# Optimization experiments

Hardware: AMD Instinct MI355X
Metric: run time of the kernel (lower is better)

## Reference

```python
import jax, jax.numpy as jnp
import numpy as np

B, N, M, C1, C2 = 16, 4096, 1024, 128, 256
MLP0, MLP1 = 256, 256
IN_CH = C1 + C2
EPS = 1e-5


def setup_inputs() -> dict:
    key = jax.random.key(0)
    ks = jax.random.split(key, 6)
    return {
        "xyz1": jax.random.normal(ks[0], (B, 3, N), jnp.float32),
        "xyz2": jax.random.normal(ks[1], (B, 3, M), jnp.float32),
        "points1": jax.random.normal(ks[2], (B, C1, N), jnp.float32),
        "points2": jax.random.normal(ks[3], (B, C2, M), jnp.float32),
        "W1": jax.random.normal(ks[4], (MLP0, IN_CH), jnp.float32) * (1.0 / np.sqrt(IN_CH)),
        "gamma1": jnp.ones((MLP0,), jnp.float32),
        "beta1": jnp.zeros((MLP0,), jnp.float32),
        "W2": jax.random.normal(ks[5], (MLP1, MLP0), jnp.float32) * (1.0 / np.sqrt(MLP0)),
        "gamma2": jnp.ones((MLP1,), jnp.float32),
        "beta2": jnp.zeros((MLP1,), jnp.float32),
    }


def _batchnorm(x, gamma, beta):
    # x: (B, N, C); normalize per channel over batch*length (training-mode BN, biased var)
    mean = jnp.mean(x, axis=(0, 1))
    var = jnp.mean((x - mean) ** 2, axis=(0, 1))
    return (x - mean) * jax.lax.rsqrt(var + EPS) * gamma + beta


def reference(xyz1, xyz2, points1, points2, W1, gamma1, beta1, W2, gamma2, beta2):
    p1 = jnp.swapaxes(xyz1, 1, 2)  # (B, N, 3)
    p2 = jnp.swapaxes(xyz2, 1, 2)  # (B, M, 3)
    # squared pairwise distances (B, N, M); squaring preserves 3-NN ordering,
    # and the original squares the euclidean dist before weighting anyway
    d2 = jnp.sum((p1[:, :, None, :] - p2[:, None, :, :]) ** 2, axis=-1)
    neg_d2, idx = jax.lax.top_k(-d2, 3)  # 3 smallest distances
    dist2 = jnp.maximum(-neg_d2, 1e-10)  # (B, N, 3)
    inv = 1.0 / dist2
    weight = inv / jnp.sum(inv, axis=-1, keepdims=True)  # (B, N, 3)
    f2 = jnp.swapaxes(points2, 1, 2)  # (B, M, C2)
    b, n, k = idx.shape
    gathered = jnp.take_along_axis(
        f2, idx.reshape(b, n * k)[:, :, None], axis=1
    ).reshape(b, n, k, -1)  # (B, N, 3, C2)
    interp = jnp.einsum("bnk,bnkc->bnc", weight, gathered)  # (B, N, C2)
    feat = jnp.concatenate([interp, jnp.swapaxes(points1, 1, 2)], axis=-1)  # (B, N, C1+C2)
    h = jnp.einsum("bnc,oc->bno", feat, W1)  # conv1d k=1, no bias
    h = jax.nn.relu(_batchnorm(h, gamma1, beta1))
    h = jnp.einsum("bnc,oc->bno", h, W2)
    h = jax.nn.relu(_batchnorm(h, gamma2, beta2))
    return jnp.swapaxes(h, 1, 2)  # (B, MLP1, N), channel-first like torch
```

## Files before the change

### kernel.cpp

```cpp
#include <hip/hip_runtime.h>

typedef unsigned short u16;
typedef unsigned int u32;

#define BB 16
#define NN 4096
#define MM 1024
#define C1V 128
#define C2V 256
#define O1 256
#define O2 256
#define EPSV 1e-5f
#define INV_CNT (1.0f/65536.0f)
#define NREP 32

typedef __attribute__((ext_vector_type(8))) short bf16x8;
typedef __attribute__((ext_vector_type(4))) float f32x4;

static __device__ __forceinline__ u16 f2b(float f) {
  u32 u = __float_as_uint(f);
  u32 r = (u + 0x7FFFu + ((u >> 16) & 1u)) >> 16;
  return (u16)r;
}
static __device__ __forceinline__ float b2f(u16 s) {
  return __uint_as_float(((u32)s) << 16);
}

#define GLD_LDS16(gp, lp)                                                      \
  __builtin_amdgcn_global_load_lds(                                            \
      (const __attribute__((address_space(1))) void*)(gp),                     \
      (__attribute__((address_space(3))) void*)(lp), 16, 0, 0)

__global__ __launch_bounds__(256) void knn_kernel(
    const float* __restrict__ xyz1, const float* __restrict__ xyz2,
    float* __restrict__ pd, int* __restrict__ pi) {
  __shared__ float4 cand[256];
  int bx = blockIdx.x;
  int c = bx & 3;
  int qt = (bx >> 2) & 7;
  int b = bx >> 5;
  int t = threadIdx.x;

  const float* x2b = xyz2 + b * 3 * MM;
  {
    float x = x2b[c * 256 + t];
    float y = x2b[MM + c * 256 + t];
    float z = x2b[2 * MM + c * 256 + t];
    cand[t] = make_float4(x, y, z, x * x + y * y + z * z);
  }
  __syncthreads();

  const float* x1b = xyz1 + b * 3 * NN;
  int n0 = qt * 512 + t;
  int n1 = n0 + 256;
  float px0 = x1b[n0], py0 = x1b[NN + n0], pz0 = x1b[2 * NN + n0];
  float px1 = x1b[n1], py1 = x1b[NN + n1], pz1 = x1b[2 * NN + n1];

  const float INF = 3.4e38f;
  float k00 = INF, k01 = INF, k02 = INF;
  float k10 = INF, k11 = INF, k12 = INF;
  int j00 = 0, j01 = 0, j02 = 0;
  int j10 = 0, j11 = 0, j12 = 0;

#pragma unroll 8
  for (int m = 0; m < 256; ++m) {
    float4 cd = cand[m];
    {
      float dot = fmaf(px0, cd.x, fmaf(py0, cd.y, pz0 * cd.z));
      float key = fmaf(-2.0f, dot, cd.w);
      bool c0 = key < k00, c1 = key < k01, c2 = key < k02;
      k02 = c1 ? k01 : (c2 ? key : k02);
      j02 = c1 ? j01 : (c2 ? m : j02);
      k01 = c0 ? k00 : (c1 ? key : k01);
      j01 = c0 ? j00 : (c1 ? m : j01);
      k00 = c0 ? key : k00;
      j00 = c0 ? m : j00;
    }
    {
      float dot = fmaf(px1, cd.x, fmaf(py1, cd.y, pz1 * cd.z));
      float key = fmaf(-2.0f, dot, cd.w);
      bool c0 = key < k10, c1 = key < k11, c2 = key < k12;
      k12 = c1 ? k11 : (c2 ? key : k12);
      j12 = c1 ? j11 : (c2 ? m : j12);
      k11 = c0 ? k10 : (c1 ? key : k11);
      j11 = c0 ? j10 : (c1 ? m : j11);
      k10 = c0 ? key : k10;
      j10 = c0 ? m : j10;
    }
  }

  float pn0 = px0 * px0 + py0 * py0 + pz0 * pz0;
  float pn1 = px1 * px1 + py1 * py1 + pz1 * pz1;
  int gq0 = b * NN + n0;
  int gq1 = b * NN + n1;
  int base = c << 8;
  ((float4*)pd)[(size_t)c * 65536 + gq0] =
      make_float4(fmaxf(k00 + pn0, 1e-10f), fmaxf(k01 + pn0, 1e-10f),
                  fmaxf(k02 + pn0, 1e-10f), 0.0f);
  ((int4*)pi)[(size_t)c * 65536 + gq0] =
      make_int4(base + j00, base + j01, base + j02, 0);
  ((float4*)pd)[(size_t)c * 65536 + gq1] =
      make_float4(fmaxf(k10 + pn1, 1e-10f), fmaxf(k11 + pn1, 1e-10f),
                  fmaxf(k12 + pn1, 1e-10f), 0.0f);
  ((int4*)pi)[(size_t)c * 65536 + gq1] =
      make_int4(base + j10, base + j11, base + j12, 0);
}

__global__ __launch_bounds__(256) void knn_merge(
    const float* __restrict__ pd, const int* __restrict__ pi,
    float* __restrict__ w_out, int* __restrict__ i_out) {
  int gq = blockIdx.x * 256 + threadIdx.x;
  float4 d0 = ((const float4*)pd)[gq];
  int4 i0 = ((const int4*)pi)[gq];
  float a0 = d0.x, a1 = d0.y, a2 = d0.z;
  int b0 = i0.x, b1 = i0.y, b2 = i0.z;
#pragma unroll
  for (int c = 1; c < 4; ++c) {
    float4 dc = ((const float4*)pd)[(size_t)c * 65536 + gq];
    int4 ic = ((const int4*)pi)[(size_t)c * 65536 + gq];
    float kv[3] = {dc.x, dc.y, dc.z};
    int jv[3] = {ic.x, ic.y, ic.z};
#pragma unroll
    for (int j = 0; j < 3; ++j) {
      float key = kv[j];
      int idx = jv[j];
      bool c0 = key < a0, c1 = key < a1, c2 = key < a2;
      a2 = c1 ? a1 : (c2 ? key : a2);
      b2 = c1 ? b1 : (c2 ? idx : b2);
      a1 = c0 ? a0 : (c1 ? key : a1);
      b1 = c0 ? b0 : (c1 ? idx : b1);
      a0 = c0 ? key : a0;
      b0 = c0 ? idx : b0;
    }
  }
  float v0 = 1.0f / a0, v1 = 1.0f / a1, v2 = 1.0f / a2;
  float s = 1.0f / (v0 + v1 + v2);
  int base = gq * 3;
  w_out[base + 0] = v0 * s;
  w_out[base + 1] = v1 * s;
  w_out[base + 2] = v2 * s;
  i_out[base + 0] = b0;
  i_out[base + 1] = b1;
  i_out[base + 2] = b2;
}

__global__ __launch_bounds__(256) void cast_w_kernel(
    const float* __restrict__ src, u16* __restrict__ dst, int n) {
  int i = blockIdx.x * 256 + threadIdx.x;
  if (i < n) dst[i] = f2b(src[i]);
}

__global__ __launch_bounds__(256) void tcast_kernel(
    const float* __restrict__ in, u16* __restrict__ out, int C, int P) {
  __shared__ float tile[32][33];
  int tx = threadIdx.x & 31, ty = threadIdx.x >> 5;
  int p0 = blockIdx.x * 32, c0 = blockIdx.y * 32, b = blockIdx.z;
  const float* ib = in + (size_t)b * C * P;
  u16* ob = out + (size_t)b * P * C;
#pragma unroll
  for (int i = 0; i < 4; ++i)
    tile[ty + i * 8][tx] = ib[(size_t)(c0 + ty + i * 8) * P + p0 + tx];
  __syncthreads();
#pragma unroll
  for (int i = 0; i < 4; ++i)
    ob[(size_t)(p0 + ty + i * 8) * C + c0 + tx] = f2b(tile[tx][ty + i * 8]);
}

__global__ __launch_bounds__(512) void stats_finalize(
    const float* __restrict__ R, float* __restrict__ outS) {
  int u = threadIdx.x;
  float s = 0.0f;
#pragma unroll
  for (int r = 0; r < NREP; ++r) s += R[r * 512 + u];
  outS[u] = s;
}

template <int K, int NTILES, bool INTERP, bool STATS, bool OUTB, bool BNA>
__global__ __launch_bounds__(256) void gemm_mfma(
    const u16* __restrict__ A, int lda, const u16* __restrict__ B, int ldb,
    void* __restrict__ out, const u16* __restrict__ G,
    const float* __restrict__ w3, const int* __restrict__ i3,
    float* __restrict__ statsOut, const float* __restrict__ statsInR,
    const float* __restrict__ gamma, const float* __restrict__ beta) {
  __shared__ u16 smem[16384];
  __shared__ float wsh[128][3];
  __shared__ int ish[128][3];
  __shared__ float scA[256], shA[256];

  int t = threadIdx.x;
  int w = t >> 6, l = t & 63;
  int n0;
  if (NTILES > 0) {
    int p = blockIdx.x;
    int batch = ((p & 7) << 1) | ((p >> 3) & 1);
    int nt = p >> 4;
    n0 = (batch * NTILES + nt) * 128;
  } else {
    n0 = blockIdx.x * 128;
  }
  int o0 = blockIdx.y * 128;

  if (INTERP) {
    for (int e = t; e < 384; e += 256) {
      int r = e / 3, j = e - 3 * r;
      wsh[r][j] = w3[(n0 + r) * 3 + j];
      ish[r][j] = i3[(n0 + r) * 3 + j];
    }
  }
  if (BNA) {
    float s = 0.0f, qq = 0.0f;
#pragma unroll
    for (int r = 0; r < NREP; ++r) {
      s += statsInR[r * 512 + t];
      qq += statsInR[r * 512 + 256 + t];
    }
    float mean = s * INV_CNT;
    float var = qq * INV_CNT - mean * mean;
    float sc = rsqrtf(var + EPSV) * gamma[t];
    scA[t] = sc;
    shA[t] = beta[t] - mean * sc;
  }

  int wm = w & 1, wn = w >> 1;
  int lr = l >> 2, lc = l & 3;
  int q = l >> 4, m = l & 15;

  f32x4 acc[4][4] = {};
  u16* As = smem;
  u16* Bs = smem + 4096;

  const u16* arow = A + (size_t)n0 * lda;
  const u16* brow = B + (size_t)o0 * ldb;

#pragma unroll
  for (int kt = 0; kt < K; kt += 32) {
    __syncthreads();
#pragma unroll
    for (int r = 0; r < 2; ++r) {
      int row = r * 64 + w * 16 + lr;
      if (BNA) {
        union { uint4 u; u16 s[8]; } v, o;
        v.u = *(const uint4*)(arow + (size_t)row * lda + kt + lc * 8);
        int cb = kt + lc * 8;
#pragma unroll
        for (int j = 0; j < 8; ++j) {
          float f = fmaf(b2f(v.s[j]), scA[cb + j], shA[cb + j]);
          o.s[j] = f2b(fmaxf(f, 0.0f));
        }
        *(uint4*)(As + row * 32 + lc * 8) = o.u;
      } else {
        GLD_LDS16(arow + (size_t)row * lda + kt + lc * 8, As + row * 32 + lc * 8);
      }
    }
#pragma unroll
    for (int r = 0; r < 2; ++r) {
      int row = r * 64 + w * 16 + lr;
      GLD_LDS16(brow + (size_t)row * ldb + kt + lc * 8, Bs + row * 32 + lc * 8);
    }
    __syncthreads();
    bf16x8 af[4], bf[4];
#pragma unroll
    for (int i = 0; i < 4; ++i)
      af[i] = *(const bf16x8*)(As + (wm * 64 + i * 16 + m) * 32 + q * 8);
#pragma unroll
    for (int j = 0; j < 4; ++j)
      bf[j] = *(const bf16x8*)(Bs + (wn * 64 + j * 16 + m) * 32 + q * 8);
#pragma unroll
    for (int i = 0; i < 4; ++i)
#pragma unroll
      for (int j = 0; j < 4; ++j)
        acc[i][j] =
            __builtin_amdgcn_mfma_f32_16x16x32_bf16(af[i], bf[j], acc[i][j], 0, 0, 0);
  }

  if (INTERP) {
    __syncthreads();
    int b = n0 >> 12;
    int rl = t >> 1, half = t & 1;
    float w0 = wsh[rl][0], w1 = wsh[rl][1], w2 = wsh[rl][2];
    const u16* g0 = G + ((size_t)(b * 1024 + ish[rl][0])) * 256 + o0 + half * 64;
    const u16* g1 = G + ((size_t)(b * 1024 + ish[rl][1])) * 256 + o0 + half * 64;
    const u16* g2 = G + ((size_t)(b * 1024 + ish[rl][2])) * 256 + o0 + half * 64;
    u16* dst = smem + rl * 128 + half * 64;
#pragma unroll
    for (int c8 = 0; c8 < 8; ++c8) {
      bf16x8 v0 = *(const bf16x8*)(g0 + c8 * 8);
      bf16x8 v1 = *(const bf16x8*)(g1 + c8 * 8);
      bf16x8 v2 = *(const bf16x8*)(g2 + c8 * 8);
      union { uint4 u; u16 s[8]; } o;
#pragma unroll
      for (int e = 0; e < 8; ++e) {
        float f = w0 * b2f((u16)v0[e]) + w1 * b2f((u16)v1[e]) +
                  w2 * b2f((u16)v2[e]);
        o.s[e] = f2b(f);
      }
      *(uint4*)(dst + c8 * 8) = o.u;
    }
    __syncthreads();
#pragma unroll
    for (int i = 0; i < 4; ++i)
#pragma unroll
      for (int reg = 0; reg < 4; ++reg) {
        int row = wm * 64 + i * 16 + q * 4 + reg;
#pragma unroll
        for (int j = 0; j < 4; ++j) {
          int col = wn * 64 + j * 16 + m;
          acc[i][j][reg] += b2f(smem[row * 128 + col]);
        }
      }
  }

  if (STATS) {
    int rep = blockIdx.x & (NREP - 1);
#pragma unroll
    for (int j = 0; j < 4; ++j) {
      float s = 0.0f, ss = 0.0f;
#pragma unroll
      for (int i = 0; i < 4; ++i)
#pragma unroll
        for (int reg = 0; reg < 4; ++reg) {
          float v = acc[i][j][reg];
          s += v;
          ss += v * v;
        }
      s += __shfl_down(s, 32); ss += __shfl_down(ss, 32);
      s += __shfl_down(s, 16); ss += __shfl_down(ss, 16);
      if (l < 16) {
        int c = o0 + wn * 64 + j * 16 + l;
        atomicAdd(&statsOut[rep * 512 + c], s);
        atomicAdd(&statsOut[rep * 512 + 256 + c], ss);
      }
    }
  }

#pragma unroll
  for (int i = 0; i < 4; ++i) {
    int gr = n0 + wm * 64 + i * 16 + q * 4;
#pragma unroll
    for (int reg = 0; reg < 4; ++reg) {
#pragma unroll
      for (int j = 0; j < 4; ++j) {
        int gc = o0 + wn * 64 + j * 16 + m;
        size_t off = (size_t)(gr + reg) * 256 + gc;
        if (OUTB)
          ((u16*)out)[off] = f2b(acc[i][j][reg]);
        else
          ((float*)out)[off] = acc[i][j][reg];
      }
    }
  }
}

__global__ __launch_bounds__(256) void bn2t_kernel(
    const u16* __restrict__ h2, const float* __restrict__ stats,
    const float* __restrict__ gamma, const float* __restrict__ beta,
    float* __restrict__ out) {
  __shared__ float tile[32][33];
  int tx = threadIdx.x & 31, ty = threadIdx.x >> 5;
  int n0 = blockIdx.x * 32, c0 = blockIdx.y * 32, b = blockIdx.z;
  int c = c0 + tx;
  float mean = stats[c] * INV_CNT;
  float var = stats[256 + c] * INV_CNT - mean * mean;
  float s = rsqrtf(var + EPSV) * gamma[c];
  float sh = beta[c] - mean * s;
#pragma unroll
  for (int i = 0; i < 4; ++i) {
    int n = n0 + ty + i * 8;
    float v = b2f(h2[((size_t)b * NN + n) * 256 + c]) * s + sh;
    tile[ty + i * 8][tx] = fmaxf(v, 0.0f);
  }
  __syncthreads();
#pragma unroll
  for (int i = 0; i < 4; ++i)
    out[((size_t)b * 256 + c0 + ty + i * 8) * NN + n0 + tx] = tile[tx][ty + i * 8];
}

extern "C" void kernel_launch(void* const* d_in, const int* in_sizes, int n_in,
                              void* d_out, int out_size, void* d_ws,
                              size_t ws_size, hipStream_t stream) {
  const float* xyz1    = (const float*)d_in[0];
  const float* xyz2    = (const float*)d_in[1];
  const float* points1 = (const float*)d_in[2];
  const float* points2 = (const float*)d_in[3];
  const float* W1      = (const float*)d_in[4];
  const float* gamma1  = (const float*)d_in[5];
  const float* beta1   = (const float*)d_in[6];
  const float* W2      = (const float*)d_in[7];
  const float* gamma2  = (const float*)d_in[8];
  const float* beta2   = (const float*)d_in[9];

  char* ws = (char*)d_ws;
  float* w3      = (float*)(ws + 0);
  int*   i3      = (int*)(ws + 786432);
  float* stats1R = (float*)(ws + 1572864);
  float* stats2R = (float*)(ws + 1638400);
  float* stats2f = (float*)(ws + 1703936);
  u16*   W1b     = (u16*)(ws + 1705984);
  u16*   W2b     = (u16*)(ws + 1902592);
  float* pd      = (float*)(ws + 2033664);
  int*   pi      = (int*)(ws + 2033664 + 4194304);
  u16*   p2t     = (u16*)(ws + 2033664);
  u16*   p1t     = (u16*)(ws + 10422272);
  u16*   G       = (u16*)(ws + 27199488);
  u16*   h2b     = (u16*)(ws + 35588096);
  u16*   h1b     = (u16*)d_out;
  float* out     = (float*)d_out;

  hipMemsetAsync(stats1R, 0, 131072, stream);
  knn_kernel<<<512, 256, 0, stream>>>(xyz1, xyz2, pd, pi);
  knn_merge<<<256, 256, 0, stream>>>(pd, pi, w3, i3);
  cast_w_kernel<<<384, 256, 0, stream>>>(W1, W1b, 98304);
  cast_w_kernel<<<256, 256, 0, stream>>>(W2, W2b, 65536);
  tcast_kernel<<<dim3(32, 8, 16), 256, 0, stream>>>(points2, p2t, C2V, MM);
  tcast_kernel<<<dim3(128, 4, 16), 256, 0, stream>>>(points1, p1t, C1V, NN);
  gemm_mfma<256, 8, false, false, true, false><<<dim3(128, 2), 256, 0, stream>>>(
      p2t, 256, W1b, 384, G, nullptr, nullptr, nullptr, nullptr, nullptr,
      nullptr, nullptr);
  gemm_mfma<128, 32, true, true, true, false><<<dim3(512, 2), 256, 0, stream>>>(
      p1t, 128, W1b + 256, 384, h1b, G, w3, i3, stats1R, nullptr, nullptr,
      nullptr);
  gemm_mfma<256, 0, false, true, true, true><<<dim3(512, 2), 256, 0, stream>>>(
      h1b, 256, W2b, 256, h2b, nullptr, nullptr, nullptr, stats2R, stats1R,
      gamma1, beta1);
  stats_finalize<<<1, 512, 0, stream>>>(stats2R, stats2f);
  bn2t_kernel<<<dim3(128, 8, 16), 256, 0, stream>>>(h2b, stats2f, gamma2,
                                                    beta2, out);
}
```

Before: 257.8 us.

## Fuse kNN merge into interp GEMM, merge weight casts, fold stats finalize, swizzle LDS

Moves the 4-way partial top-3 merge and inverse-distance weighting into the prologue of the interpolation GEMM, so the separate knn_merge kernel and its w3/i3 round trip go away. The two weight-cast launches become one, and the stats_finalize kernel is removed by having bn2t reduce the per-replica stats itself. The gathered interpolation tile in shared memory now uses an XOR swizzle to cut bank conflicts. The costs are that the merge runs twice (once per o-block, blockIdx.y=2) and bn2t re-sums 32 replicas in every block. The workspace layout is also reshuffled.

```diff
diff --git a/kernel.cpp b/kernel.cpp
--- a/kernel.cpp
+++ b/kernel.cpp
@@ -106,48 +106,12 @@
       make_int4(base + j10, base + j11, base + j12, 0);
 }
 
-__global__ __launch_bounds__(256) void knn_merge(
-    const float* __restrict__ pd, const int* __restrict__ pi,
-    float* __restrict__ w_out, int* __restrict__ i_out) {
-  int gq = blockIdx.x * 256 + threadIdx.x;
-  float4 d0 = ((const float4*)pd)[gq];
-  int4 i0 = ((const int4*)pi)[gq];
-  float a0 = d0.x, a1 = d0.y, a2 = d0.z;
-  int b0 = i0.x, b1 = i0.y, b2 = i0.z;
-#pragma unroll
-  for (int c = 1; c < 4; ++c) {
-    float4 dc = ((const float4*)pd)[(size_t)c * 65536 + gq];
-    int4 ic = ((const int4*)pi)[(size_t)c * 65536 + gq];
-    float kv[3] = {dc.x, dc.y, dc.z};
-    int jv[3] = {ic.x, ic.y, ic.z};
-#pragma unroll
-    for (int j = 0; j < 3; ++j) {
-      float key = kv[j];
-      int idx = jv[j];
-      bool c0 = key < a0, c1 = key < a1, c2 = key < a2;
-      a2 = c1 ? a1 : (c2 ? key : a2);
-      b2 = c1 ? b1 : (c2 ? idx : b2);
-      a1 = c0 ? a0 : (c1 ? key : a1);
-      b1 = c0 ? b0 : (c1 ? idx : b1);
-      a0 = c0 ? key : a0;
-      b0 = c0 ? idx : b0;
-    }
-  }
-  float v0 = 1.0f / a0, v1 = 1.0f / a1, v2 = 1.0f / a2;
-  float s = 1.0f / (v0 + v1 + v2);
-  int base = gq * 3;
-  w_out[base + 0] = v0 * s;
-  w_out[base + 1] = v1 * s;
-  w_out[base + 2] = v2 * s;
-  i_out[base + 0] = b0;
-  i_out[base + 1] = b1;
-  i_out[base + 2] = b2;
-}
-
 __global__ __launch_bounds__(256) void cast_w_kernel(
-    const float* __restrict__ src, u16* __restrict__ dst, int n) {
+    const float* __restrict__ W1, const float* __restrict__ W2,
+    u16* __restrict__ d1, u16* __restrict__ d2) {
   int i = blockIdx.x * 256 + threadIdx.x;
-  if (i < n) dst[i] = f2b(src[i]);
+  if (i < 98304) d1[i] = f2b(W1[i]);
+  else if (i < 163840) d2[i - 98304] = f2b(W2[i - 98304]);
 }
 
 __global__ __launch_bounds__(256) void tcast_kernel(
@@ -166,20 +130,11 @@
     ob[(size_t)(p0 + ty + i * 8) * C + c0 + tx] = f2b(tile[tx][ty + i * 8]);
 }
 
-__global__ __launch_bounds__(512) void stats_finalize(
-    const float* __restrict__ R, float* __restrict__ outS) {
-  int u = threadIdx.x;
-  float s = 0.0f;
-#pragma unroll
-  for (int r = 0; r < NREP; ++r) s += R[r * 512 + u];
-  outS[u] = s;
-}
-
 template <int K, int NTILES, bool INTERP, bool STATS, bool OUTB, bool BNA>
 __global__ __launch_bounds__(256) void gemm_mfma(
     const u16* __restrict__ A, int lda, const u16* __restrict__ B, int ldb,
     void* __restrict__ out, const u16* __restrict__ G,
-    const float* __restrict__ w3, const int* __restrict__ i3,
+    const float* __restrict__ pd, const int* __restrict__ pi,
     float* __restrict__ statsOut, const float* __restrict__ statsInR,
     const float* __restrict__ gamma, const float* __restrict__ beta) {
   __shared__ u16 smem[16384];
@@ -201,10 +156,35 @@
   int o0 = blockIdx.y * 128;
 
   if (INTERP) {
-    for (int e = t; e < 384; e += 256) {
-      int r = e / 3, j = e - 3 * r;
-      wsh[r][j] = w3[(n0 + r) * 3 + j];
-      ish[r][j] = i3[(n0 + r) * 3 + j];
+    if (t < 128) {
+      int gq = n0 + t;
+      float4 d0 = ((const float4*)pd)[gq];
+      int4 ii0 = ((const int4*)pi)[gq];
+      float a0 = d0.x, a1 = d0.y, a2 = d0.z;
+      int b0 = ii0.x, b1 = ii0.y, b2 = ii0.z;
+#pragma unroll
+      for (int c = 1; c < 4; ++c) {
+        float4 dc = ((const float4*)pd)[(size_t)c * 65536 + gq];
+        int4 ic = ((const int4*)pi)[(size_t)c * 65536 + gq];
+        float kv[3] = {dc.x, dc.y, dc.z};
+        int jv[3] = {ic.x, ic.y, ic.z};
+#pragma unroll
+        for (int j = 0; j < 3; ++j) {
+          float key = kv[j];
+          int idx = jv[j];
+          bool c0 = key < a0, c1 = key < a1, c2 = key < a2;
+          a2 = c1 ? a1 : (c2 ? key : a2);
+          b2 = c1 ? b1 : (c2 ? idx : b2);
+          a1 = c0 ? a0 : (c1 ? key : a1);
+          b1 = c0 ? b0 : (c1 ? idx : b1);
+          a0 = c0 ? key : a0;
+          b0 = c0 ? idx : b0;
+        }
+      }
+      float v0 = 1.0f / a0, v1 = 1.0f / a1, v2 = 1.0f / a2;
+      float s = 1.0f / (v0 + v1 + v2);
+      wsh[t][0] = v0 * s; wsh[t][1] = v1 * s; wsh[t][2] = v2 * s;
+      ish[t][0] = b0;     ish[t][1] = b1;     ish[t][2] = b2;
     }
   }
   if (BNA) {
@@ -276,12 +256,11 @@
   if (INTERP) {
     __syncthreads();
     int b = n0 >> 12;
-    int rl = t >> 1, half = t & 1;
+    int rl = t >> 1, half = t & 1, rx = rl & 7;
     float w0 = wsh[rl][0], w1 = wsh[rl][1], w2 = wsh[rl][2];
     const u16* g0 = G + ((size_t)(b * 1024 + ish[rl][0])) * 256 + o0 + half * 64;
     const u16* g1 = G + ((size_t)(b * 1024 + ish[rl][1])) * 256 + o0 + half * 64;
     const u16* g2 = G + ((size_t)(b * 1024 + ish[rl][2])) * 256 + o0 + half * 64;
-    u16* dst = smem + rl * 128 + half * 64;
 #pragma unroll
     for (int c8 = 0; c8 < 8; ++c8) {
       bf16x8 v0 = *(const bf16x8*)(g0 + c8 * 8);
@@ -294,7 +273,8 @@
                   w2 * b2f((u16)v2[e]);
         o.s[e] = f2b(f);
       }
-      *(uint4*)(dst + c8 * 8) = o.u;
+      int ch = (half * 8 + c8) ^ rx;
+      *(uint4*)(smem + rl * 128 + ch * 8) = o.u;
     }
     __syncthreads();
 #pragma unroll
@@ -302,10 +282,12 @@
 #pragma unroll
       for (int reg = 0; reg < 4; ++reg) {
         int row = wm * 64 + i * 16 + q * 4 + reg;
+        int rxr = row & 7;
 #pragma unroll
         for (int j = 0; j < 4; ++j) {
           int col = wn * 64 + j * 16 + m;
-          acc[i][j][reg] += b2f(smem[row * 128 + col]);
+          int off = row * 128 + (((col >> 3) ^ rxr) << 3) + (col & 7);
+          acc[i][j][reg] += b2f(smem[off]);
         }
       }
   }
@@ -352,21 +334,33 @@
 }
 
 __global__ __launch_bounds__(256) void bn2t_kernel(
-    const u16* __restrict__ h2, const float* __restrict__ stats,
+    const u16* __restrict__ h2, const float* __restrict__ statsR,
     const float* __restrict__ gamma, const float* __restrict__ beta,
     float* __restrict__ out) {
   __shared__ float tile[32][33];
-  int tx = threadIdx.x & 31, ty = threadIdx.x >> 5;
+  __shared__ float sS[32], sH[32];
+  int t = threadIdx.x;
+  int tx = t & 31, ty = t >> 5;
   int n0 = blockIdx.x * 32, c0 = blockIdx.y * 32, b = blockIdx.z;
-  int c = c0 + tx;
-  float mean = stats[c] * INV_CNT;
-  float var = stats[256 + c] * INV_CNT - mean * mean;
-  float s = rsqrtf(var + EPSV) * gamma[c];
-  float sh = beta[c] - mean * s;
+  if (t < 32) {
+    int c = c0 + t;
+    float s = 0.0f, qq = 0.0f;
+#pragma unroll
+    for (int r = 0; r < NREP; ++r) {
+      s += statsR[r * 512 + c];
+      qq += statsR[r * 512 + 256 + c];
+    }
+    float mean = s * INV_CNT;
+    float var = qq * INV_CNT - mean * mean;
+    float sc = rsqrtf(var + EPSV) * gamma[c];
+    sS[t] = sc;
+    sH[t] = beta[c] - mean * sc;
+  }
+  __syncthreads();
 #pragma unroll
   for (int i = 0; i < 4; ++i) {
     int n = n0 + ty + i * 8;
-    float v = b2f(h2[((size_t)b * NN + n) * 256 + c]) * s + sh;
+    float v = b2f(h2[((size_t)b * NN + n) * 256 + c0 + tx]) * sS[tx] + sH[tx];
     tile[ty + i * 8][tx] = fmaxf(v, 0.0f);
   }
   __syncthreads();
@@ -390,39 +384,33 @@
   const float* beta2   = (const float*)d_in[9];
 
   char* ws = (char*)d_ws;
-  float* w3      = (float*)(ws + 0);
-  int*   i3      = (int*)(ws + 786432);
-  float* stats1R = (float*)(ws + 1572864);
-  float* stats2R = (float*)(ws + 1638400);
-  float* stats2f = (float*)(ws + 1703936);
-  u16*   W1b     = (u16*)(ws + 1705984);
-  u16*   W2b     = (u16*)(ws + 1902592);
-  float* pd      = (float*)(ws + 2033664);
-  int*   pi      = (int*)(ws + 2033664 + 4194304);
-  u16*   p2t     = (u16*)(ws + 2033664);
-  u16*   p1t     = (u16*)(ws + 10422272);
-  u16*   G       = (u16*)(ws + 27199488);
-  u16*   h2b     = (u16*)(ws + 35588096);
+  float* stats1R = (float*)(ws + 0);
+  float* stats2R = (float*)(ws + 65536);
+  u16*   W1b     = (u16*)(ws + 131072);
+  u16*   W2b     = (u16*)(ws + 327680);
+  u16*   p2t     = (u16*)(ws + 458752);
+  u16*   p1t     = (u16*)(ws + 8847360);
+  u16*   G       = (u16*)(ws + 25624576);
+  u16*   h2b     = (u16*)(ws + 34013184);
+  float* pd      = (float*)(ws + 67567616);
+  int*   pi      = (int*)(ws + 71761920);
   u16*   h1b     = (u16*)d_out;
   float* out     = (float*)d_out;
 
   hipMemsetAsync(stats1R, 0, 131072, stream);
   knn_kernel<<<512, 256, 0, stream>>>(xyz1, xyz2, pd, pi);
-  knn_merge<<<256, 256, 0, stream>>>(pd, pi, w3, i3);
-  cast_w_kernel<<<384, 256, 0, stream>>>(W1, W1b, 98304);
-  cast_w_kernel<<<256, 256, 0, stream>>>(W2, W2b, 65536);
+  cast_w_kernel<<<640, 256, 0, stream>>>(W1, W2, W1b, W2b);
   tcast_kernel<<<dim3(32, 8, 16), 256, 0, stream>>>(points2, p2t, C2V, MM);
   tcast_kernel<<<dim3(128, 4, 16), 256, 0, stream>>>(points1, p1t, C1V, NN);
   gemm_mfma<256, 8, false, false, true, false><<<dim3(128, 2), 256, 0, stream>>>(
       p2t, 256, W1b, 384, G, nullptr, nullptr, nullptr, nullptr, nullptr,
       nullptr, nullptr);
   gemm_mfma<128, 32, true, true, true, false><<<dim3(512, 2), 256, 0, stream>>>(
-      p1t, 128, W1b + 256, 384, h1b, G, w3, i3, stats1R, nullptr, nullptr,
+      p1t, 128, W1b + 256, 384, h1b, G, pd, pi, stats1R, nullptr, nullptr,
       nullptr);
   gemm_mfma<256, 0, false, true, true, true><<<dim3(512, 2), 256, 0, stream>>>(
       h1b, 256, W2b, 256, h2b, nullptr, nullptr, nullptr, stats2R, stats1R,
       gamma1, beta1);
-  stats_finalize<<<1, 512, 0, stream>>>(stats2R, stats2f);
-  bn2t_kernel<<<dim3(128, 8, 16), 256, 0, stream>>>(h2b, stats2f, gamma2,
+  bn2t_kernel<<<dim3(128, 8, 16), 256, 0, stream>>>(h2b, stats2R, gamma2,
                                                     beta2, out);
 }
```

New measurement: 251.3 us. -2.5%, faster.
